# Optimization experiments

Measured on AMD Instinct MI355X. Metric: run time of the kernel, lower is better.

Reference implementation:

```python
import jax, jax.numpy as jnp
import numpy as np

B, S, H, F, E, K = 4, 2048, 1024, 2048, 8, 2  # batch, seq, hidden, ffn, experts, top_k


def setup_inputs() -> dict:
    key = jax.random.key(0)
    k0, k1, k2, k3, k4 = jax.random.split(key, 5)
    return {
        "hidden_states": jax.random.normal(k0, (B, S, H), dtype=jnp.float32),
        "w_router": jax.random.normal(k1, (H, E), dtype=jnp.float32) * 0.02,
        "w0": jax.random.normal(k2, (E, H, F), dtype=jnp.float32) * 0.02,  # gate_proj
        "w1": jax.random.normal(k3, (E, H, F), dtype=jnp.float32) * 0.02,  # up_proj
        "wo": jax.random.normal(k4, (E, F, H), dtype=jnp.float32) * 0.02,  # down_proj
    }


def reference(hidden_states, w_router, w0, w1, wo):
    """MoE: router top-k + softmax over selected logits, gated-FFN experts, weighted combine."""
    b, s, h = hidden_states.shape
    e = w_router.shape[1]
    x = hidden_states.reshape(-1, h)                      # [T, H], T = b*s
    t = x.shape[0]

    router_logits = x @ w_router                          # [T, E]
    top_w, top_i = jax.lax.top_k(router_logits, K)        # [T, K]
    top_w = jax.nn.softmax(top_w.astype(jnp.float32), axis=-1).astype(x.dtype)

    # Dense combine weights [T, E]: scatter top-k softmax weights to expert slots.
    gating = jnp.zeros((t, e), dtype=x.dtype).at[
        jnp.arange(t)[:, None], top_i
    ].add(top_w)

    # Per-expert gated FFN (loop over small fixed expert count), combine with gating.
    out = jnp.zeros_like(x)
    for ei in range(e):
        hmid = jax.nn.silu(x @ w0[ei]) * (x @ w1[ei])     # [T, F]
        out = out + gating[:, ei:ei + 1] * (hmid @ wo[ei])
    return out.reshape(b, s, h)
```

## Files before the change

kernel.cpp:

```cpp
#include <hip/hip_runtime.h>
#include <hip/hip_bf16.h>

#define NT 8192
#define NH 1024
#define NF 2048
#define NE 8
#define NROWS (NT * 2)

typedef short bf16x8 __attribute__((ext_vector_type(8)));
typedef float f32x4 __attribute__((ext_vector_type(4)));

__device__ __forceinline__ void gload16(const void* g, void* l) {
  __builtin_amdgcn_global_load_lds(
      (const __attribute__((address_space(1))) unsigned int*)g,
      (__attribute__((address_space(3))) unsigned int*)l, 16, 0, 0);
}

__device__ __forceinline__ unsigned short f2bf(float f) {
  __hip_bfloat16 h = __float2bfloat16(f);
  return *reinterpret_cast<unsigned short*>(&h);
}

__global__ void k_convert_x(const float* __restrict__ in, unsigned short* __restrict__ out) {
  const int i = blockIdx.x * blockDim.x + threadIdx.x;
  const float4 v = reinterpret_cast<const float4*>(in)[i];
  ushort4 u;
  u.x = f2bf(v.x); u.y = f2bf(v.y); u.z = f2bf(v.z); u.w = f2bf(v.w);
  reinterpret_cast<ushort4*>(out)[i] = u;
}

__global__ void k_transpose_convert(const float* __restrict__ in, unsigned short* __restrict__ out,
                                    int R, int C) {
  __shared__ float tile[32][33];
  const int e = blockIdx.z;
  const int c0 = blockIdx.x * 32, r0 = blockIdx.y * 32;
  const float* src = in + (size_t)e * R * C;
  unsigned short* dst = out + (size_t)e * R * C;
  const int tx = threadIdx.x, ty = threadIdx.y;
#pragma unroll
  for (int i = 0; i < 4; ++i)
    tile[ty + 8 * i][tx] = src[(size_t)(r0 + ty + 8 * i) * C + (c0 + tx)];
  __syncthreads();
#pragma unroll
  for (int i = 0; i < 4; ++i)
    dst[(size_t)(c0 + ty + 8 * i) * R + (r0 + tx)] = f2bf(tile[tx][ty + 8 * i]);
}

__global__ void k_router(const float* __restrict__ x, const float* __restrict__ wrt,
                         int* __restrict__ top_e, float* __restrict__ top_w,
                         int* __restrict__ cnt) {
  const int t = blockIdx.x * 4 + (threadIdx.x >> 6);
  const int lane = threadIdx.x & 63;
  const float* xr = x + (size_t)t * NH;
  float acc[NE];
#pragma unroll
  for (int e = 0; e < NE; ++e) acc[e] = 0.f;
  for (int h = lane; h < NH; h += 64) {
    const float xv = xr[h];
    const float4 wa = *reinterpret_cast<const float4*>(&wrt[h * NE]);
    const float4 wb = *reinterpret_cast<const float4*>(&wrt[h * NE + 4]);
    acc[0] += xv * wa.x; acc[1] += xv * wa.y; acc[2] += xv * wa.z; acc[3] += xv * wa.w;
    acc[4] += xv * wb.x; acc[5] += xv * wb.y; acc[6] += xv * wb.z; acc[7] += xv * wb.w;
  }
#pragma unroll
  for (int e = 0; e < NE; ++e)
#pragma unroll
    for (int off = 32; off > 0; off >>= 1) acc[e] += __shfl_xor(acc[e], off, 64);
  if (lane == 0) {
    int e0 = 0; float l0 = acc[0];
#pragma unroll
    for (int e = 1; e < NE; ++e) if (acc[e] > l0) { l0 = acc[e]; e0 = e; }
    int e1 = -1; float l1 = -3.4e38f;
#pragma unroll
    for (int e = 0; e < NE; ++e) if (e != e0 && acc[e] > l1) { l1 = acc[e]; e1 = e; }
    const float ex = expf(l1 - l0);
    const float s = 1.f / (1.f + ex);
    top_e[t * 2 + 0] = e0; top_e[t * 2 + 1] = e1;
    top_w[t * 2 + 0] = s;  top_w[t * 2 + 1] = ex * s;
    atomicAdd(&cnt[e0], 1); atomicAdd(&cnt[e1], 1);
  }
}

__global__ void k_prefix(const int* __restrict__ cnt, int* __restrict__ base,
                         int* __restrict__ cursor) {
  if (threadIdx.x == 0 && blockIdx.x == 0) {
    int s = 0;
    for (int e = 0; e < NE; ++e) { base[e] = s; cursor[e] = s; s += cnt[e]; }
    base[NE] = s;
  }
}

__global__ void k_scatter(const int* __restrict__ top_e, const float* __restrict__ top_w,
                          int* __restrict__ cursor, int* __restrict__ rowmap,
                          float* __restrict__ roww) {
  const int t = blockIdx.x * blockDim.x + threadIdx.x;
  if (t >= NT) return;
#pragma unroll
  for (int k = 0; k < 2; ++k) {
    const int e = top_e[t * 2 + k];
    const int pos = atomicAdd(&cursor[e], 1);
    rowmap[pos] = t;
    roww[pos] = top_w[t * 2 + k];
  }
}

__launch_bounds__(256, 2)
__global__ void k_gemm1(const unsigned short* __restrict__ xb,
                        const unsigned short* __restrict__ w0t,
                        const unsigned short* __restrict__ w1t,
                        unsigned short* __restrict__ hmid,
                        const int* __restrict__ rowmap,
                        const int* __restrict__ ebase,
                        const int* __restrict__ ecnt) {
  const int e = blockIdx.z;
  const int cnt = ecnt[e];
  const int rt = blockIdx.x, nt = blockIdx.y;
  if (rt * 128 >= cnt) return;
  __shared__ __align__(16) unsigned short As[128 * 64];
  __shared__ __align__(16) unsigned short B0s[128 * 64];
  __shared__ __align__(16) unsigned short B1s[128 * 64];
  const int tid = threadIdx.x;
  const int lane = tid & 63, wid = tid >> 6;
  const int eb = ebase[e];
  const int rsub = lane >> 3;
  const int csub = (lane & 7) * 8;

  const unsigned short* ap[4];
  const unsigned short* b0p[4];
  const unsigned short* b1p[4];
#pragma unroll
  for (int i = 0; i < 4; ++i) {
    const int r = (wid * 4 + i) * 8 + rsub;
    int lr = rt * 128 + r;
    if (lr >= cnt) lr = cnt - 1;
    const int tok = rowmap[eb + lr];
    ap[i] = xb + (size_t)tok * NH + csub;
    const int n = nt * 128 + r;
    b0p[i] = w0t + ((size_t)e * NF + n) * NH + csub;
    b1p[i] = w1t + ((size_t)e * NF + n) * NH + csub;
  }
  const int wr = wid >> 1, wn = wid & 1;
  f32x4 acc0[4][4] = {};
  f32x4 acc1[4][4] = {};

  for (int kh = 0; kh < NH; kh += 64) {
    __syncthreads();
#pragma unroll
    for (int i = 0; i < 4; ++i) gload16(ap[i] + kh, &As[(wid * 4 + i) * 8 * 64]);
#pragma unroll
    for (int i = 0; i < 4; ++i) gload16(b0p[i] + kh, &B0s[(wid * 4 + i) * 8 * 64]);
#pragma unroll
    for (int i = 0; i < 4; ++i) gload16(b1p[i] + kh, &B1s[(wid * 4 + i) * 8 * 64]);
    __syncthreads();
#pragma unroll
    for (int ks = 0; ks < 2; ++ks) {
      const int ko = ks * 32 + (lane >> 4) * 8;
      bf16x8 a[4], b0[4], b1[4];
#pragma unroll
      for (int mi = 0; mi < 4; ++mi)
        a[mi] = *reinterpret_cast<const bf16x8*>(&As[(wr * 64 + mi * 16 + (lane & 15)) * 64 + ko]);
#pragma unroll
      for (int ni = 0; ni < 4; ++ni) {
        b0[ni] = *reinterpret_cast<const bf16x8*>(&B0s[(wn * 64 + ni * 16 + (lane & 15)) * 64 + ko]);
        b1[ni] = *reinterpret_cast<const bf16x8*>(&B1s[(wn * 64 + ni * 16 + (lane & 15)) * 64 + ko]);
      }
#pragma unroll
      for (int mi = 0; mi < 4; ++mi)
#pragma unroll
        for (int ni = 0; ni < 4; ++ni) {
          acc0[mi][ni] = __builtin_amdgcn_mfma_f32_16x16x32_bf16(a[mi], b0[ni], acc0[mi][ni], 0, 0, 0);
          acc1[mi][ni] = __builtin_amdgcn_mfma_f32_16x16x32_bf16(a[mi], b1[ni], acc1[mi][ni], 0, 0, 0);
        }
    }
  }
#pragma unroll
  for (int mi = 0; mi < 4; ++mi)
#pragma unroll
    for (int ni = 0; ni < 4; ++ni)
#pragma unroll
      for (int r = 0; r < 4; ++r) {
        const int lr = rt * 128 + wr * 64 + mi * 16 + (lane >> 4) * 4 + r;
        if (lr >= cnt) continue;
        const int col = nt * 128 + wn * 64 + ni * 16 + (lane & 15);
        const float g = acc0[mi][ni][r], u = acc1[mi][ni][r];
        const float hv = g / (1.f + __expf(-g)) * u;
        hmid[(size_t)(eb + lr) * NF + col] = f2bf(hv);
      }
}

__launch_bounds__(256, 2)
__global__ void k_gemm2(const unsigned short* __restrict__ hmid,
                        const unsigned short* __restrict__ wot,
                        float* __restrict__ out,
                        const int* __restrict__ rowmap,
                        const float* __restrict__ roww,
                        const int* __restrict__ ebase,
                        const int* __restrict__ ecnt) {
  const int e = blockIdx.z;
  const int cnt = ecnt[e];
  const int rt = blockIdx.x, nt = blockIdx.y;
  if (rt * 128 >= cnt) return;
  __shared__ __align__(16) unsigned short As[128 * 64];
  __shared__ __align__(16) unsigned short Bs[128 * 64];
  const int tid = threadIdx.x;
  const int lane = tid & 63, wid = tid >> 6;
  const int eb = ebase[e];
  const int rsub = lane >> 3;
  const int csub = (lane & 7) * 8;
  const unsigned short* ap[4];
  const unsigned short* bp[4];
#pragma unroll
  for (int i = 0; i < 4; ++i) {
    const int r = (wid * 4 + i) * 8 + rsub;
    int lr = rt * 128 + r;
    if (lr >= cnt) lr = cnt - 1;
    ap[i] = hmid + (size_t)(eb + lr) * NF + csub;
    const int n = nt * 128 + r;
    bp[i] = wot + ((size_t)e * NH + n) * NF + csub;
  }
  const int wr = wid >> 1, wn = wid & 1;
  f32x4 acc[4][4] = {};

  for (int kf = 0; kf < NF; kf += 64) {
    __syncthreads();
#pragma unroll
    for (int i = 0; i < 4; ++i) gload16(ap[i] + kf, &As[(wid * 4 + i) * 8 * 64]);
#pragma unroll
    for (int i = 0; i < 4; ++i) gload16(bp[i] + kf, &Bs[(wid * 4 + i) * 8 * 64]);
    __syncthreads();
#pragma unroll
    for (int ks = 0; ks < 2; ++ks) {
      const int ko = ks * 32 + (lane >> 4) * 8;
      bf16x8 a[4], b[4];
#pragma unroll
      for (int mi = 0; mi < 4; ++mi)
        a[mi] = *reinterpret_cast<const bf16x8*>(&As[(wr * 64 + mi * 16 + (lane & 15)) * 64 + ko]);
#pragma unroll
      for (int ni = 0; ni < 4; ++ni)
        b[ni] = *reinterpret_cast<const bf16x8*>(&Bs[(wn * 64 + ni * 16 + (lane & 15)) * 64 + ko]);
#pragma unroll
      for (int mi = 0; mi < 4; ++mi)
#pragma unroll
        for (int ni = 0; ni < 4; ++ni)
          acc[mi][ni] = __builtin_amdgcn_mfma_f32_16x16x32_bf16(a[mi], b[ni], acc[mi][ni], 0, 0, 0);
    }
  }
#pragma unroll
  for (int mi = 0; mi < 4; ++mi)
#pragma unroll
    for (int ni = 0; ni < 4; ++ni)
#pragma unroll
      for (int r = 0; r < 4; ++r) {
        const int lr = rt * 128 + wr * 64 + mi * 16 + (lane >> 4) * 4 + r;
        if (lr >= cnt) continue;
        const int prow = eb + lr;
        const int tok = rowmap[prow];
        const float w = roww[prow];
        const int col = nt * 128 + wn * 64 + ni * 16 + (lane & 15);
        unsafeAtomicAdd(&out[(size_t)tok * NH + col], acc[mi][ni][r] * w);
      }
}

extern "C" void kernel_launch(void* const* d_in, const int* in_sizes, int n_in,
                              void* d_out, int out_size, void* d_ws, size_t ws_size,
                              hipStream_t stream) {
  const float* x   = (const float*)d_in[0];
  const float* wrt = (const float*)d_in[1];
  const float* w0  = (const float*)d_in[2];
  const float* w1  = (const float*)d_in[3];
  const float* wo  = (const float*)d_in[4];
  float* out = (float*)d_out;

  char* ws = (char*)d_ws;
  size_t off = 0;
  auto carve = [&](size_t bytes) -> char* {
    char* p = ws + off;
    off = (off + bytes + 255) & ~(size_t)255;
    return p;
  };
  unsigned short* xb   = (unsigned short*)carve((size_t)NT * NH * 2);
  unsigned short* w0t  = (unsigned short*)carve((size_t)NE * NF * NH * 2);
  unsigned short* w1t  = (unsigned short*)carve((size_t)NE * NF * NH * 2);
  unsigned short* wot  = (unsigned short*)carve((size_t)NE * NH * NF * 2);
  unsigned short* hmid = (unsigned short*)carve((size_t)NROWS * NF * 2);
  int*   rowmap = (int*)carve(NROWS * 4);
  float* roww   = (float*)carve(NROWS * 4);
  int*   top_e  = (int*)carve(NT * 2 * 4);
  float* top_w  = (float*)carve(NT * 2 * 4);
  int*   cnt    = (int*)carve(256);
  int*   base   = (int*)carve(256);
  int*   cursor = (int*)carve(256);
  if (off > ws_size) return;

  hipMemsetAsync(cnt, 0, 256, stream);
  hipMemsetAsync(out, 0, (size_t)out_size * sizeof(float), stream);

  k_convert_x<<<(NT * NH / 4) / 256, 256, 0, stream>>>(x, xb);
  k_transpose_convert<<<dim3(NF / 32, NH / 32, NE), dim3(32, 8), 0, stream>>>(w0, w0t, NH, NF);
  k_transpose_convert<<<dim3(NF / 32, NH / 32, NE), dim3(32, 8), 0, stream>>>(w1, w1t, NH, NF);
  k_transpose_convert<<<dim3(NH / 32, NF / 32, NE), dim3(32, 8), 0, stream>>>(wo, wot, NF, NH);

  k_router<<<NT / 4, 256, 0, stream>>>(x, wrt, top_e, top_w, cnt);
  k_prefix<<<1, 64, 0, stream>>>(cnt, base, cursor);
  k_scatter<<<NT / 256, 256, 0, stream>>>(top_e, top_w, cursor, rowmap, roww);

  k_gemm1<<<dim3(64, NF / 128, NE), 256, 0, stream>>>(xb, w0t, w1t, hmid, rowmap, base, cnt);
  k_gemm2<<<dim3(64, NH / 128, NE), 256, 0, stream>>>(hmid, wot, out, rowmap, roww, base, cnt);
}
```

Before: 1.080 ms.

## Split fused gate/up GEMM into two passes to halve accumulator registers

Replaces the fused gate+up GEMM, which held two 4x4 accumulator tiles per wave, with a single templated GEMM run twice. The up projection is written to hmid in bf16, then the gate pass reads it back and applies SiLU*up in its epilogue. This halves accumulator register and LDS pressure so occupancy can rise. In exchange it loads the gathered x tiles twice, adds an extra round trip of the intermediate through global memory, and rounds the up product to bf16 before the multiply.

```diff
diff --git a/kernel.cpp b/kernel.cpp
--- a/kernel.cpp
+++ b/kernel.cpp
@@ -104,101 +104,21 @@
   }
 }
 
+template <int MODE>
 __launch_bounds__(256, 2)
-__global__ void k_gemm1(const unsigned short* __restrict__ xb,
-                        const unsigned short* __restrict__ w0t,
-                        const unsigned short* __restrict__ w1t,
-                        unsigned short* __restrict__ hmid,
-                        const int* __restrict__ rowmap,
-                        const int* __restrict__ ebase,
-                        const int* __restrict__ ecnt) {
+__global__ void k_gemm(const unsigned short* __restrict__ Aglob,
+                       const unsigned short* __restrict__ Bglob,
+                       unsigned short* __restrict__ hmid,
+                       float* __restrict__ out,
+                       const int* __restrict__ rowmap,
+                       const float* __restrict__ roww,
+                       const int* __restrict__ ebase,
+                       const int* __restrict__ ecnt) {
+  constexpr int KDIM = (MODE == 2) ? NF : NH;
+  constexpr int BROWS = (MODE == 2) ? NH : NF;
   const int e = blockIdx.z;
   const int cnt = ecnt[e];
-  const int rt = blockIdx.x, nt = blockIdx.y;
-  if (rt * 128 >= cnt) return;
-  __shared__ __align__(16) unsigned short As[128 * 64];
-  __shared__ __align__(16) unsigned short B0s[128 * 64];
-  __shared__ __align__(16) unsigned short B1s[128 * 64];
-  const int tid = threadIdx.x;
-  const int lane = tid & 63, wid = tid >> 6;
-  const int eb = ebase[e];
-  const int rsub = lane >> 3;
-  const int csub = (lane & 7) * 8;
-
-  const unsigned short* ap[4];
-  const unsigned short* b0p[4];
-  const unsigned short* b1p[4];
-#pragma unroll
-  for (int i = 0; i < 4; ++i) {
-    const int r = (wid * 4 + i) * 8 + rsub;
-    int lr = rt * 128 + r;
-    if (lr >= cnt) lr = cnt - 1;
-    const int tok = rowmap[eb + lr];
-    ap[i] = xb + (size_t)tok * NH + csub;
-    const int n = nt * 128 + r;
-    b0p[i] = w0t + ((size_t)e * NF + n) * NH + csub;
-    b1p[i] = w1t + ((size_t)e * NF + n) * NH + csub;
-  }
-  const int wr = wid >> 1, wn = wid & 1;
-  f32x4 acc0[4][4] = {};
-  f32x4 acc1[4][4] = {};
-
-  for (int kh = 0; kh < NH; kh += 64) {
-    __syncthreads();
-#pragma unroll
-    for (int i = 0; i < 4; ++i) gload16(ap[i] + kh, &As[(wid * 4 + i) * 8 * 64]);
-#pragma unroll
-    for (int i = 0; i < 4; ++i) gload16(b0p[i] + kh, &B0s[(wid * 4 + i) * 8 * 64]);
-#pragma unroll
-    for (int i = 0; i < 4; ++i) gload16(b1p[i] + kh, &B1s[(wid * 4 + i) * 8 * 64]);
-    __syncthreads();
-#pragma unroll
-    for (int ks = 0; ks < 2; ++ks) {
-      const int ko = ks * 32 + (lane >> 4) * 8;
-      bf16x8 a[4], b0[4], b1[4];
-#pragma unroll
-      for (int mi = 0; mi < 4; ++mi)
-        a[mi] = *reinterpret_cast<const bf16x8*>(&As[(wr * 64 + mi * 16 + (lane & 15)) * 64 + ko]);
-#pragma unroll
-      for (int ni = 0; ni < 4; ++ni) {
-        b0[ni] = *reinterpret_cast<const bf16x8*>(&B0s[(wn * 64 + ni * 16 + (lane & 15)) * 64 + ko]);
-        b1[ni] = *reinterpret_cast<const bf16x8*>(&B1s[(wn * 64 + ni * 16 + (lane & 15)) * 64 + ko]);
-      }
-#pragma unroll
-      for (int mi = 0; mi < 4; ++mi)
-#pragma unroll
-        for (int ni = 0; ni < 4; ++ni) {
-          acc0[mi][ni] = __builtin_amdgcn_mfma_f32_16x16x32_bf16(a[mi], b0[ni], acc0[mi][ni], 0, 0, 0);
-          acc1[mi][ni] = __builtin_amdgcn_mfma_f32_16x16x32_bf16(a[mi], b1[ni], acc1[mi][ni], 0, 0, 0);
-        }
-    }
-  }
-#pragma unroll
-  for (int mi = 0; mi < 4; ++mi)
-#pragma unroll
-    for (int ni = 0; ni < 4; ++ni)
-#pragma unroll
-      for (int r = 0; r < 4; ++r) {
-        const int lr = rt * 128 + wr * 64 + mi * 16 + (lane >> 4) * 4 + r;
-        if (lr >= cnt) continue;
-        const int col = nt * 128 + wn * 64 + ni * 16 + (lane & 15);
-        const float g = acc0[mi][ni][r], u = acc1[mi][ni][r];
-        const float hv = g / (1.f + __expf(-g)) * u;
-        hmid[(size_t)(eb + lr) * NF + col] = f2bf(hv);
-      }
-}
-
-__launch_bounds__(256, 2)
-__global__ void k_gemm2(const unsigned short* __restrict__ hmid,
-                        const unsigned short* __restrict__ wot,
-                        float* __restrict__ out,
-                        const int* __restrict__ rowmap,
-                        const float* __restrict__ roww,
-                        const int* __restrict__ ebase,
-                        const int* __restrict__ ecnt) {
-  const int e = blockIdx.z;
-  const int cnt = ecnt[e];
-  const int rt = blockIdx.x, nt = blockIdx.y;
+  const int rt = blockIdx.x, ntb = blockIdx.y;
   if (rt * 128 >= cnt) return;
   __shared__ __align__(16) unsigned short As[128 * 64];
   __shared__ __align__(16) unsigned short Bs[128 * 64];
@@ -207,6 +127,7 @@
   const int eb = ebase[e];
   const int rsub = lane >> 3;
   const int csub = (lane & 7) * 8;
+
   const unsigned short* ap[4];
   const unsigned short* bp[4];
 #pragma unroll
@@ -214,19 +135,24 @@
     const int r = (wid * 4 + i) * 8 + rsub;
     int lr = rt * 128 + r;
     if (lr >= cnt) lr = cnt - 1;
-    ap[i] = hmid + (size_t)(eb + lr) * NF + csub;
-    const int n = nt * 128 + r;
-    bp[i] = wot + ((size_t)e * NH + n) * NF + csub;
+    if (MODE == 2) {
+      ap[i] = Aglob + (size_t)(eb + lr) * KDIM + csub;
+    } else {
+      const int tok = rowmap[eb + lr];
+      ap[i] = Aglob + (size_t)tok * KDIM + csub;
+    }
+    const int n = ntb * 128 + r;
+    bp[i] = Bglob + ((size_t)e * BROWS + n) * KDIM + csub;
   }
   const int wr = wid >> 1, wn = wid & 1;
   f32x4 acc[4][4] = {};
 
-  for (int kf = 0; kf < NF; kf += 64) {
+  for (int kk = 0; kk < KDIM; kk += 64) {
     __syncthreads();
 #pragma unroll
-    for (int i = 0; i < 4; ++i) gload16(ap[i] + kf, &As[(wid * 4 + i) * 8 * 64]);
-#pragma unroll
-    for (int i = 0; i < 4; ++i) gload16(bp[i] + kf, &Bs[(wid * 4 + i) * 8 * 64]);
+    for (int i = 0; i < 4; ++i) gload16(ap[i] + kk, &As[(wid * 4 + i) * 8 * 64]);
+#pragma unroll
+    for (int i = 0; i < 4; ++i) gload16(bp[i] + kk, &Bs[(wid * 4 + i) * 8 * 64]);
     __syncthreads();
 #pragma unroll
     for (int ks = 0; ks < 2; ++ks) {
@@ -245,6 +171,7 @@
           acc[mi][ni] = __builtin_amdgcn_mfma_f32_16x16x32_bf16(a[mi], b[ni], acc[mi][ni], 0, 0, 0);
     }
   }
+
 #pragma unroll
   for (int mi = 0; mi < 4; ++mi)
 #pragma unroll
@@ -253,11 +180,18 @@
       for (int r = 0; r < 4; ++r) {
         const int lr = rt * 128 + wr * 64 + mi * 16 + (lane >> 4) * 4 + r;
         if (lr >= cnt) continue;
-        const int prow = eb + lr;
-        const int tok = rowmap[prow];
-        const float w = roww[prow];
-        const int col = nt * 128 + wn * 64 + ni * 16 + (lane & 15);
-        unsafeAtomicAdd(&out[(size_t)tok * NH + col], acc[mi][ni][r] * w);
+        const int col = ntb * 128 + wn * 64 + ni * 16 + (lane & 15);
+        if (MODE == 0) {
+          hmid[(size_t)(eb + lr) * NF + col] = f2bf(acc[mi][ni][r]);
+        } else if (MODE == 1) {
+          const size_t idx = (size_t)(eb + lr) * NF + col;
+          const float g = acc[mi][ni][r];
+          const float u = __bfloat162float(*reinterpret_cast<const __hip_bfloat16*>(&hmid[idx]));
+          hmid[idx] = f2bf(g / (1.f + __expf(-g)) * u);
+        } else {
+          const int prow = eb + lr;
+          unsafeAtomicAdd(&out[(size_t)rowmap[prow] * NH + col], acc[mi][ni][r] * roww[prow]);
+        }
       }
 }
 
@@ -304,6 +238,7 @@
   k_prefix<<<1, 64, 0, stream>>>(cnt, base, cursor);
   k_scatter<<<NT / 256, 256, 0, stream>>>(top_e, top_w, cursor, rowmap, roww);
 
-  k_gemm1<<<dim3(64, NF / 128, NE), 256, 0, stream>>>(xb, w0t, w1t, hmid, rowmap, base, cnt);
-  k_gemm2<<<dim3(64, NH / 128, NE), 256, 0, stream>>>(hmid, wot, out, rowmap, roww, base, cnt);
-}
+  k_gemm<0><<<dim3(64, NF / 128, NE), 256, 0, stream>>>(xb, w1t, hmid, nullptr, rowmap, nullptr, base, cnt);
+  k_gemm<1><<<dim3(64, NF / 128, NE), 256, 0, stream>>>(xb, w0t, hmid, nullptr, rowmap, nullptr, base, cnt);
+  k_gemm<2><<<dim3(64, NH / 128, NE), 256, 0, stream>>>(hmid, wot, nullptr, out, rowmap, roww, base, cnt);
+}
```

Measured after the change: 1.179 ms. 9.1% more time.
